# Optimization experiments

Hardware: AMD Instinct MI355X
Metric: run time of the kernel (lower is better)

The kernel has to match this reference:

```python
import jax, jax.numpy as jnp
import numpy as np

E = 8      # num routed experts
H = 1024   # hidden_size
I = 1408   # moe_intermediate_size
T = 2048   # tokens (batch*seq flattened)
K = 2      # top_k experts per token


def setup_inputs() -> dict:
    key = jax.random.key(0)
    k1, k2, k3, k4, k5 = jax.random.split(key, 5)
    x = jax.random.normal(k1, (T, H), dtype=jnp.float32)
    expert_ids = jax.random.randint(k2, (T, K), 0, E, dtype=jnp.int64)
    routing_weights = jax.random.uniform(k3, (T, K), dtype=jnp.float32)
    # kaiming_uniform_(a=sqrt(5)) on 2D tensor -> bound = 1/sqrt(fan_in), fan_in = dim1
    b1 = 1.0 / np.sqrt(2 * I)
    w1 = jax.random.uniform(k4, (E * H, 2 * I), dtype=jnp.float32, minval=-b1, maxval=b1)
    b2 = 1.0 / np.sqrt(H)
    w2 = jax.random.uniform(k5, (E * I, H), dtype=jnp.float32, minval=-b2, maxval=b2)
    return {"x": x, "expert_ids": expert_ids, "routing_weights": routing_weights,
            "w1": w1, "w2": w2}


def reference(x, expert_ids, routing_weights, w1, w2):
    # Fused routed MLP: per token, for each of its top-k experts e with gate p:
    #   out += p * (silu(x @ W1_gate[e]) * (x @ W1_up[e])) @ W2[e]
    w1r = w1.reshape(E, H, 2 * I)   # fused gate+up per expert
    w2r = w2.reshape(E, I, H)       # down proj per expert

    h = jnp.einsum('th,ehi->eti', x, w1r)           # [E, T, 2I]
    gate, up = h[..., :I], h[..., I:]
    act = jax.nn.silu(gate) * up                    # [E, T, I]
    y = jnp.einsum('eti,eih->eth', act, w2r)        # [E, T, H]

    # combine weights: [T, E] = sum over the k slots of onehot(expert)*routing_weight
    disp = jnp.sum(jax.nn.one_hot(expert_ids, E, dtype=x.dtype)
                   * routing_weights[..., None], axis=1)  # [T, E]
    out = jnp.einsum('eth,te->th', y, disp)         # [T, H]
    return out
```

## Files before the change

kernel.cpp:

```cpp
#include <hip/hip_runtime.h>
#include <hip/hip_bf16.h>
#include <math.h>

#define E    8
#define H    1024
#define I2   2816
#define II   1408
#define T    2048
#define KTOP 2
#define NP   (T * KTOP)

#define BM   128
#define BK   32
#define BNA  64
#define BN2  128
#define GX   40
#define GXT  8

#define CVT_BLKS  1024
#define W1_TILES  (16 * 44 * E)
#define PREP_BLKS (1 + CVT_BLKS + W1_TILES)

#define W2_TILES     2816
#define W2_BLOCKS    (GXT * 22)
#define W2_PER_BLOCK (W2_TILES / W2_BLOCKS)

typedef __attribute__((ext_vector_type(8))) short  short8v;
typedef __attribute__((ext_vector_type(4))) float  f32x4;
typedef __attribute__((ext_vector_type(8))) unsigned short ushort8;

__device__ __forceinline__ void gload16(void* lds, const void* g) {
    __builtin_amdgcn_global_load_lds((const __attribute__((address_space(1))) unsigned int*)g,
                                     (__attribute__((address_space(3))) unsigned int*)lds,
                                     16, 0, 0);
}

__device__ __forceinline__ void transpose_tile_async(
    const float* __restrict__ src, __hip_bfloat16* __restrict__ dst,
    int K, int N, int k0, int n0, float* tile, int tid)
{
    int lane = tid & 63;
    int wv   = tid >> 6;
#pragma unroll
    for (int i = 0; i < 4; ++i) {
        int q   = (wv * 4 + i) * 64 + lane;
        int r   = q >> 4;
        int c16 = q & 15;
        const float* gsrc = src + (size_t)(k0 + r) * N + n0 + ((c16 ^ (r & 15)) << 2);
        gload16(tile + q * 4, gsrc);
    }
    __syncthreads();

    int n  = tid >> 2;
    int ks = (tid & 3) * 16;
    alignas(16) __hip_bfloat16 t[16];
#pragma unroll
    for (int j = 0; j < 16; ++j) {
        int r = ks + j;
        float v = tile[r * 64 + (((n >> 2) ^ (r & 15)) << 2) + (n & 3)];
        t[j] = __float2bfloat16(v);
    }
    __hip_bfloat16* d = dst + (size_t)(n0 + n) * K + k0 + ks;
    *(ushort8*)(d)     = ((ushort8*)t)[0];
    *(ushort8*)(d + 8) = ((ushort8*)t)[1];
}

union PrepShared {
    float tile[4096];
    struct { int cnt4[4][E]; int woff[4][E]; } rt;
};

__launch_bounds__(256)
__global__ void prep_kernel(const float* __restrict__ x, const float* __restrict__ w1,
                            const int* __restrict__ ids,
                            __hip_bfloat16* __restrict__ xb,
                            __hip_bfloat16* __restrict__ w1t,
                            int* __restrict__ tok, int* __restrict__ inv,
                            int* __restrict__ seg_off, int* __restrict__ tile_off)
{
    __shared__ __align__(16) PrepShared sh;
    int tid = threadIdx.x;
    int b = blockIdx.x;

    if (b == 0) {
        int lane = tid & 63;
        int w    = tid >> 6;
        unsigned long long ltm = (1ull << lane) - 1ull;

        int wc = 0;
#pragma unroll 1
        for (int it = 0; it < 16; ++it) {
            int p = it * 256 + w * 64 + lane;
            int e = ids[p];
#pragma unroll
            for (int ee = 0; ee < E; ++ee) {
                unsigned long long m = __ballot(e == ee);
                if (lane == ee) wc += (int)__popcll(m);
            }
        }
        if (lane < E) sh.rt.cnt4[w][lane] = wc;
        __syncthreads();
        if (tid == 0) {
            int base = 0, tiles = 0;
            for (int e = 0; e < E; ++e) {
                seg_off[e]  = base;
                tile_off[e] = tiles;
                int tot = 0;
                for (int ww = 0; ww < 4; ++ww) {
                    sh.rt.woff[ww][e] = base + tot;
                    tot += sh.rt.cnt4[ww][e];
                }
                base  += tot;
                tiles += (tot + BM - 1) / BM;
            }
            seg_off[E]  = base;
            tile_off[E] = tiles;
        }
        __syncthreads();
        int run = (lane < E) ? sh.rt.woff[w][lane] : 0;
#pragma unroll 1
        for (int it = 0; it < 16; ++it) {
            int p = it * 256 + w * 64 + lane;
            int e = ids[p];
            unsigned long long me = 0;
            int acnt = 0;
#pragma unroll
            for (int ee = 0; ee < E; ++ee) {
                unsigned long long m = __ballot(e == ee);
                if (e == ee) me = m;
                if (lane == ee) acnt = (int)__popcll(m);
            }
            int rank = (int)__popcll(me & ltm);
            int qb   = __shfl(run, e, 64);
            int q    = qb + rank;
            tok[q] = p >> 1;
            inv[p] = q;
            run += acnt;
        }
        return;
    }
    b -= 1;

    if (b < CVT_BLKS) {
        int i = (b * 256 + tid) * 8;
        float4 a = *(const float4*)(x + i);
        float4 c = *(const float4*)(x + i + 4);
        alignas(16) __hip_bfloat16 t[8];
        t[0] = __float2bfloat16(a.x); t[1] = __float2bfloat16(a.y);
        t[2] = __float2bfloat16(a.z); t[3] = __float2bfloat16(a.w);
        t[4] = __float2bfloat16(c.x); t[5] = __float2bfloat16(c.y);
        t[6] = __float2bfloat16(c.z); t[7] = __float2bfloat16(c.w);
        *(ushort8*)(xb + i) = *(ushort8*)t;
        return;
    }
    b -= CVT_BLKS;

    {
        int e = b / 704, r = b % 704;
        int k0 = (r / 44) * 64, n0 = (r % 44) * 64;
        transpose_tile_async(w1 + (size_t)e * H * I2, w1t + (size_t)e * I2 * H,
                             H, I2, k0, n0, sh.tile, tid);
    }
}

union Gemm1Shared {
    struct {
        __hip_bfloat16 As[BM * BK];
        __hip_bfloat16 Bg[BNA * BK];
        __hip_bfloat16 Bu[BNA * BK];
        int tokS[BM];
    } g;
    float tile[4096];
};

__launch_bounds__(256, 2)
__global__ void gemm1_silu(const __hip_bfloat16* __restrict__ xb,
                           const __hip_bfloat16* __restrict__ w1t,
                           const float* __restrict__ w2,
                           __hip_bfloat16* __restrict__ w2t,
                           const int* __restrict__ tok,
                           const int* __restrict__ seg_off,
                           const int* __restrict__ tile_off,
                           __hip_bfloat16* __restrict__ act)
{
    __shared__ __align__(16) Gemm1Shared sh;
    int tid = threadIdx.x;
    int bx = blockIdx.x;

    if (bx >= GX) {
        int wid = (bx - GX) * 22 + blockIdx.y;
#pragma unroll 1
        for (int i = 0; i < W2_PER_BLOCK; ++i) {
            int t = wid * W2_PER_BLOCK + i;
            int e = t / 352, r = t % 352;
            int k0 = (r >> 4) * 64, n0 = (r & 15) * 64;
            transpose_tile_async(w2 + (size_t)e * II * H, w2t + (size_t)e * H * II,
                                 II, H, k0, n0, sh.tile, tid);
            __syncthreads();
        }
        return;
    }

    if (bx >= tile_off[E]) return;
    int e = 0;
#pragma unroll
    for (int i = 1; i < E; ++i) if (bx >= tile_off[i]) e = i;
    int row0 = seg_off[e] + (bx - tile_off[e]) * BM;
    int rend = seg_off[e + 1];
    int jb   = blockIdx.y * BNA;

    __hip_bfloat16* As = sh.g.As;
    __hip_bfloat16* Bg = sh.g.Bg;
    __hip_bfloat16* Bu = sh.g.Bu;

    if (tid < BM) {
        int gr = row0 + tid;
        sh.g.tokS[tid] = tok[gr < NP ? gr : NP - 1];
    }
    __syncthreads();

    int arow = tid >> 2;
    int aoff = (tid & 3) * 16;
    const char* xB  = (const char*)xb;
    const char* w1B = (const char*)(w1t + (size_t)e * I2 * H);
    const char* srcA0 = xB + (size_t)sh.g.tokS[arow]      * 2048 + aoff;
    const char* srcA1 = xB + (size_t)sh.g.tokS[arow + 64] * 2048 + aoff;
    const char* srcG  = w1B + (size_t)(jb + arow)      * 2048 + aoff;
    const char* srcU  = w1B + (size_t)(II + jb + arow) * 2048 + aoff;
    __hip_bfloat16* dA0 = &As[tid * 8];
    __hip_bfloat16* dA1 = &As[2048 + tid * 8];
    __hip_bfloat16* dG  = &Bg[tid * 8];
    __hip_bfloat16* dU  = &Bu[tid * 8];

    int lane = tid & 63;
    int w  = tid >> 6;
    int wm = w >> 1, wn = w & 1;
    int fr = lane & 15;
    int kc = lane >> 4;

    f32x4 accg[4][2] = {};
    f32x4 accu[4][2] = {};
    const short8v* Asv = (const short8v*)As;
    const short8v* Bgv = (const short8v*)Bg;
    const short8v* Buv = (const short8v*)Bu;

    for (int k0 = 0; k0 < H; k0 += BK) {
        gload16(dA0, srcA0);
        gload16(dA1, srcA1);
        gload16(dG, srcG);
        gload16(dU, srcU);
        srcA0 += 64; srcA1 += 64; srcG += 64; srcU += 64;
        __syncthreads();

        short8v a[4], g[2], u[2];
#pragma unroll
        for (int m = 0; m < 4; ++m)
            a[m] = Asv[(wm * 64 + m * 16 + fr) * 4 + kc];
#pragma unroll
        for (int n = 0; n < 2; ++n) {
            g[n] = Bgv[(wn * 32 + n * 16 + fr) * 4 + kc];
            u[n] = Buv[(wn * 32 + n * 16 + fr) * 4 + kc];
        }
#pragma unroll
        for (int m = 0; m < 4; ++m)
#pragma unroll
            for (int n = 0; n < 2; ++n) {
                accg[m][n] = __builtin_amdgcn_mfma_f32_16x16x32_bf16(a[m], g[n], accg[m][n], 0, 0, 0);
                accu[m][n] = __builtin_amdgcn_mfma_f32_16x16x32_bf16(a[m], u[n], accu[m][n], 0, 0, 0);
            }
        __syncthreads();
    }

#pragma unroll
    for (int m = 0; m < 4; ++m)
#pragma unroll
        for (int n = 0; n < 2; ++n) {
            int col = jb + wn * 32 + n * 16 + fr;
#pragma unroll
            for (int j = 0; j < 4; ++j) {
                int gr = row0 + wm * 64 + m * 16 + kc * 4 + j;
                if (gr < rend) {
                    float gg = accg[m][n][j];
                    float s  = gg / (1.0f + __expf(-gg));
                    act[(size_t)gr * II + col] = __float2bfloat16(s * accu[m][n][j]);
                }
            }
        }
}

__launch_bounds__(256, 2)
__global__ void gemm2(const __hip_bfloat16* __restrict__ act,
                      const __hip_bfloat16* __restrict__ w2t,
                      const int* __restrict__ seg_off,
                      const int* __restrict__ tile_off,
                      float* __restrict__ y)
{
    __shared__ __align__(16) __hip_bfloat16 As[BM * BK];
    __shared__ __align__(16) __hip_bfloat16 Bs[BN2 * BK];

    int bx = blockIdx.x;
    if (bx >= tile_off[E]) return;
    int e = 0;
#pragma unroll
    for (int i = 1; i < E; ++i) if (bx >= tile_off[i]) e = i;
    int row0 = seg_off[e] + (bx - tile_off[e]) * BM;
    int rend = seg_off[e + 1];
    int nb   = blockIdx.y * BN2;

    int tid = threadIdx.x;
    int arow = tid >> 2;
    int aoff = (tid & 3) * 16;
    const char* actB = (const char*)act;
    const char* w2B  = (const char*)(w2t + (size_t)e * H * II);
    int r0c = row0 + arow;       r0c = r0c < NP ? r0c : NP - 1;
    int r1c = row0 + arow + 64;  r1c = r1c < NP ? r1c : NP - 1;
    const char* srcA0 = actB + (size_t)r0c * 2816 + aoff;
    const char* srcA1 = actB + (size_t)r1c * 2816 + aoff;
    const char* srcB0 = w2B + (size_t)(nb + arow)      * 2816 + aoff;
    const char* srcB1 = w2B + (size_t)(nb + arow + 64) * 2816 + aoff;
    __hip_bfloat16* dA0 = &As[tid * 8];
    __hip_bfloat16* dA1 = &As[2048 + tid * 8];
    __hip_bfloat16* dB0 = &Bs[tid * 8];
    __hip_bfloat16* dB1 = &Bs[2048 + tid * 8];

    int lane = tid & 63;
    int w  = tid >> 6;
    int wm = w >> 1, wn = w & 1;
    int fr = lane & 15;
    int kc = lane >> 4;

    f32x4 acc[4][4] = {};
    const short8v* Asv = (const short8v*)As;
    const short8v* Bsv = (const short8v*)Bs;

    for (int k0 = 0; k0 < II; k0 += BK) {
        gload16(dA0, srcA0);
        gload16(dA1, srcA1);
        gload16(dB0, srcB0);
        gload16(dB1, srcB1);
        srcA0 += 64; srcA1 += 64; srcB0 += 64; srcB1 += 64;
        __syncthreads();

        short8v a[4], b[4];
#pragma unroll
        for (int m = 0; m < 4; ++m)
            a[m] = Asv[(wm * 64 + m * 16 + fr) * 4 + kc];
#pragma unroll
        for (int n = 0; n < 4; ++n)
            b[n] = Bsv[(wn * 64 + n * 16 + fr) * 4 + kc];
#pragma unroll
        for (int m = 0; m < 4; ++m)
#pragma unroll
            for (int n = 0; n < 4; ++n)
                acc[m][n] = __builtin_amdgcn_mfma_f32_16x16x32_bf16(a[m], b[n], acc[m][n], 0, 0, 0);
        __syncthreads();
    }

#pragma unroll
    for (int m = 0; m < 4; ++m)
#pragma unroll
        for (int n = 0; n < 4; ++n) {
            int col = nb + wn * 64 + n * 16 + fr;
#pragma unroll
            for (int j = 0; j < 4; ++j) {
                int lr = wm * 64 + m * 16 + kc * 4 + j;
                int gr = row0 + lr;
                if (gr < rend)
                    y[(size_t)gr * H + col] = acc[m][n][j];
            }
        }
}

__global__ void gather_out(const float* __restrict__ y, const int* __restrict__ inv,
                           const float* __restrict__ rw, float* __restrict__ out)
{
    int gid = blockIdx.x * 256 + threadIdx.x;
    int t = gid >> 8;
    int c = (gid & 255) * 4;
    int q0 = inv[2 * t], q1 = inv[2 * t + 1];
    float w0 = rw[2 * t], w1 = rw[2 * t + 1];
    float4 a = *(const float4*)(y + (size_t)q0 * H + c);
    float4 b = *(const float4*)(y + (size_t)q1 * H + c);
    float4 o;
    o.x = w0 * a.x + w1 * b.x;
    o.y = w0 * a.y + w1 * b.y;
    o.z = w0 * a.z + w1 * b.z;
    o.w = w0 * a.w + w1 * b.w;
    *(float4*)(out + (size_t)t * H + c) = o;
}

extern "C" void kernel_launch(void* const* d_in, const int* in_sizes, int n_in,
                              void* d_out, int out_size, void* d_ws, size_t ws_size,
                              hipStream_t stream)
{
    const float* x   = (const float*)d_in[0];
    const int*   ids = (const int*)d_in[1];
    const float* rw  = (const float*)d_in[2];
    const float* w1  = (const float*)d_in[3];
    const float* w2  = (const float*)d_in[4];
    float*       out = (float*)d_out;

    char* ws = (char*)d_ws;
    int*   tok  = (int*)ws;
    int*   inv  = (int*)(ws + 16384);
    int*   seg  = (int*)(ws + 32768);
    int*   tile = (int*)(ws + 32768 + 64);
    __hip_bfloat16* xb  = (__hip_bfloat16*)(ws + 65536);
    __hip_bfloat16* w1t = (__hip_bfloat16*)(ws + 4259840);
    __hip_bfloat16* w2t = (__hip_bfloat16*)(ws + 50397184);
    __hip_bfloat16* act = (__hip_bfloat16*)(ws + 73465856);
    float*          y   = (float*)(ws + 85000192);

    prep_kernel<<<PREP_BLKS, 256, 0, stream>>>(x, w1, ids, xb, w1t, tok, inv, seg, tile);

    gemm1_silu<<<dim3(GX + GXT, II / BNA), 256, 0, stream>>>(xb, w1t, w2, w2t,
                                                             tok, seg, tile, act);
    gemm2<<<dim3(GX, H / BN2), 256, 0, stream>>>(act, w2t, seg, tile, y);
    gather_out<<<(T * H) / (256 * 4), 256, 0, stream>>>(y, inv, rw, out);
}
```

Before: 285.3 us.

## Double-buffer LDS tiles with async prefetch in GEMMs and weight transposes

Converts the gemm1, gemm2 and w2-transpose loops to double-buffered LDS staging. The next k-slice is issued with global_load_lds before the current one is consumed, using s_waitcnt vmcnt(4) and a raw barrier instead of __syncthreads. The prep kernel now handles two W1 transpose tiles per block so the second load overlaps the first tile's processing. The aim is to hide global-load latency behind MFMA and convert work. The cost is double the LDS footprint, which can lower occupancy. Correctness also depends on hand-counted vmcnt values matching the compiler's load ordering.

```diff
diff --git a/kernel.cpp b/kernel.cpp
--- a/kernel.cpp
+++ b/kernel.cpp
@@ -17,9 +17,10 @@
 #define GX   40
 #define GXT  8
 
-#define CVT_BLKS  1024
-#define W1_TILES  (16 * 44 * E)
-#define PREP_BLKS (1 + CVT_BLKS + W1_TILES)
+#define CVT_BLKS   1024
+#define W1_TILES   (16 * 44 * E)
+#define W1_BLKS    (W1_TILES / 2)
+#define PREP_BLKS  (1 + CVT_BLKS + W1_BLKS)
 
 #define W2_TILES     2816
 #define W2_BLOCKS    (GXT * 22)
@@ -28,6 +29,10 @@
 typedef __attribute__((ext_vector_type(8))) short  short8v;
 typedef __attribute__((ext_vector_type(4))) float  f32x4;
 typedef __attribute__((ext_vector_type(8))) unsigned short ushort8;
+
+#define VMCNT4() asm volatile("s_waitcnt vmcnt(4)" ::: "memory")
+#define VMCNT0() asm volatile("s_waitcnt vmcnt(0)" ::: "memory")
+#define BAR()    __builtin_amdgcn_s_barrier()
 
 __device__ __forceinline__ void gload16(void* lds, const void* g) {
     __builtin_amdgcn_global_load_lds((const __attribute__((address_space(1))) unsigned int*)g,
@@ -35,9 +40,8 @@
                                      16, 0, 0);
 }
 
-__device__ __forceinline__ void transpose_tile_async(
-    const float* __restrict__ src, __hip_bfloat16* __restrict__ dst,
-    int K, int N, int k0, int n0, float* tile, int tid)
+__device__ __forceinline__ void tr_issue(const float* __restrict__ src, int N,
+                                         int k0, int n0, float* tile, int tid)
 {
     int lane = tid & 63;
     int wv   = tid >> 6;
@@ -46,19 +50,21 @@
         int q   = (wv * 4 + i) * 64 + lane;
         int r   = q >> 4;
         int c16 = q & 15;
-        const float* gsrc = src + (size_t)(k0 + r) * N + n0 + ((c16 ^ (r & 15)) << 2);
-        gload16(tile + q * 4, gsrc);
-    }
-    __syncthreads();
-
+        gload16(tile + q * 4, src + (size_t)(k0 + r) * N + n0 + ((c16 ^ (r & 15)) << 2));
+    }
+}
+
+__device__ __forceinline__ void tr_process(const float* tile,
+                                           __hip_bfloat16* __restrict__ dst,
+                                           int K, int k0, int n0, int tid)
+{
     int n  = tid >> 2;
     int ks = (tid & 3) * 16;
     alignas(16) __hip_bfloat16 t[16];
 #pragma unroll
     for (int j = 0; j < 16; ++j) {
         int r = ks + j;
-        float v = tile[r * 64 + (((n >> 2) ^ (r & 15)) << 2) + (n & 3)];
-        t[j] = __float2bfloat16(v);
+        t[j] = __float2bfloat16(tile[r * 64 + (((n >> 2) ^ (r & 15)) << 2) + (n & 3)]);
     }
     __hip_bfloat16* d = dst + (size_t)(n0 + n) * K + k0 + ks;
     *(ushort8*)(d)     = ((ushort8*)t)[0];
@@ -66,7 +72,7 @@
 }
 
 union PrepShared {
-    float tile[4096];
+    float tile[2][4096];
     struct { int cnt4[4][E]; int woff[4][E]; } rt;
 };
 
@@ -156,21 +162,34 @@
     b -= CVT_BLKS;
 
     {
-        int e = b / 704, r = b % 704;
-        int k0 = (r / 44) * 64, n0 = (r % 44) * 64;
-        transpose_tile_async(w1 + (size_t)e * H * I2, w1t + (size_t)e * I2 * H,
-                             H, I2, k0, n0, sh.tile, tid);
+        int t0 = b * 2, t1 = b * 2 + 1;
+        int e0 = t0 / 704, r0 = t0 % 704;
+        int e1 = t1 / 704, r1 = t1 % 704;
+        const float*    s0 = w1  + (size_t)e0 * H * I2;
+        const float*    s1 = w1  + (size_t)e1 * H * I2;
+        __hip_bfloat16* d0 = w1t + (size_t)e0 * I2 * H;
+        __hip_bfloat16* d1 = w1t + (size_t)e1 * I2 * H;
+        int k00 = (r0 / 44) * 64, n00 = (r0 % 44) * 64;
+        int k01 = (r1 / 44) * 64, n01 = (r1 % 44) * 64;
+        tr_issue(s0, I2, k00, n00, sh.tile[0], tid);
+        tr_issue(s1, I2, k01, n01, sh.tile[1], tid);
+        VMCNT4();
+        BAR();
+        tr_process(sh.tile[0], d0, H, k00, n00, tid);
+        VMCNT0();
+        BAR();
+        tr_process(sh.tile[1], d1, H, k01, n01, tid);
     }
 }
 
 union Gemm1Shared {
     struct {
-        __hip_bfloat16 As[BM * BK];
-        __hip_bfloat16 Bg[BNA * BK];
-        __hip_bfloat16 Bu[BNA * BK];
+        __hip_bfloat16 As[2][BM * BK];
+        __hip_bfloat16 Bg[2][BNA * BK];
+        __hip_bfloat16 Bu[2][BNA * BK];
         int tokS[BM];
     } g;
-    float tile[4096];
+    float tile[2][4096];
 };
 
 __launch_bounds__(256, 2)
@@ -189,14 +208,33 @@
 
     if (bx >= GX) {
         int wid = (bx - GX) * 22 + blockIdx.y;
+        int tbase = wid * W2_PER_BLOCK;
+        {
+            int t = tbase;
+            int e = t / 352, r = t % 352;
+            tr_issue(w2 + (size_t)e * II * H, H, (r >> 4) * 64, (r & 15) * 64,
+                     sh.tile[0], tid);
+        }
 #pragma unroll 1
         for (int i = 0; i < W2_PER_BLOCK; ++i) {
-            int t = wid * W2_PER_BLOCK + i;
-            int e = t / 352, r = t % 352;
-            int k0 = (r >> 4) * 64, n0 = (r & 15) * 64;
-            transpose_tile_async(w2 + (size_t)e * II * H, w2t + (size_t)e * H * II,
-                                 II, H, k0, n0, sh.tile, tid);
-            __syncthreads();
+            int cur = i & 1;
+            if (i < W2_PER_BLOCK - 1) {
+                int t = tbase + i + 1;
+                int e = t / 352, r = t % 352;
+                tr_issue(w2 + (size_t)e * II * H, H, (r >> 4) * 64, (r & 15) * 64,
+                         sh.tile[cur ^ 1], tid);
+                VMCNT4();
+            } else {
+                VMCNT0();
+            }
+            BAR();
+            {
+                int t = tbase + i;
+                int e = t / 352, r = t % 352;
+                tr_process(sh.tile[cur], w2t + (size_t)e * H * II, II,
+                           (r >> 4) * 64, (r & 15) * 64, tid);
+            }
+            BAR();
         }
         return;
     }
@@ -208,10 +246,6 @@
     int row0 = seg_off[e] + (bx - tile_off[e]) * BM;
     int rend = seg_off[e + 1];
     int jb   = blockIdx.y * BNA;
-
-    __hip_bfloat16* As = sh.g.As;
-    __hip_bfloat16* Bg = sh.g.Bg;
-    __hip_bfloat16* Bu = sh.g.Bu;
 
     if (tid < BM) {
         int gr = row0 + tid;
@@ -227,10 +261,6 @@
     const char* srcA1 = xB + (size_t)sh.g.tokS[arow + 64] * 2048 + aoff;
     const char* srcG  = w1B + (size_t)(jb + arow)      * 2048 + aoff;
     const char* srcU  = w1B + (size_t)(II + jb + arow) * 2048 + aoff;
-    __hip_bfloat16* dA0 = &As[tid * 8];
-    __hip_bfloat16* dA1 = &As[2048 + tid * 8];
-    __hip_bfloat16* dG  = &Bg[tid * 8];
-    __hip_bfloat16* dU  = &Bu[tid * 8];
 
     int lane = tid & 63;
     int w  = tid >> 6;
@@ -240,18 +270,31 @@
 
     f32x4 accg[4][2] = {};
     f32x4 accu[4][2] = {};
-    const short8v* Asv = (const short8v*)As;
-    const short8v* Bgv = (const short8v*)Bg;
-    const short8v* Buv = (const short8v*)Bu;
-
-    for (int k0 = 0; k0 < H; k0 += BK) {
-        gload16(dA0, srcA0);
-        gload16(dA1, srcA1);
-        gload16(dG, srcG);
-        gload16(dU, srcU);
-        srcA0 += 64; srcA1 += 64; srcG += 64; srcU += 64;
-        __syncthreads();
-
+
+    gload16(&sh.g.As[0][tid * 8], srcA0);
+    gload16(&sh.g.As[0][2048 + tid * 8], srcA1);
+    gload16(&sh.g.Bg[0][tid * 8], srcG);
+    gload16(&sh.g.Bu[0][tid * 8], srcU);
+    srcA0 += 64; srcA1 += 64; srcG += 64; srcU += 64;
+
+#pragma unroll 1
+    for (int t = 0; t < H / BK; ++t) {
+        int cur = t & 1;
+        if (t < H / BK - 1) {
+            gload16(&sh.g.As[cur ^ 1][tid * 8], srcA0);
+            gload16(&sh.g.As[cur ^ 1][2048 + tid * 8], srcA1);
+            gload16(&sh.g.Bg[cur ^ 1][tid * 8], srcG);
+            gload16(&sh.g.Bu[cur ^ 1][tid * 8], srcU);
+            srcA0 += 64; srcA1 += 64; srcG += 64; srcU += 64;
+            VMCNT4();
+        } else {
+            VMCNT0();
+        }
+        BAR();
+
+        const short8v* Asv = (const short8v*)sh.g.As[cur];
+        const short8v* Bgv = (const short8v*)sh.g.Bg[cur];
+        const short8v* Buv = (const short8v*)sh.g.Bu[cur];
         short8v a[4], g[2], u[2];
 #pragma unroll
         for (int m = 0; m < 4; ++m)
@@ -268,7 +311,7 @@
                 accg[m][n] = __builtin_amdgcn_mfma_f32_16x16x32_bf16(a[m], g[n], accg[m][n], 0, 0, 0);
                 accu[m][n] = __builtin_amdgcn_mfma_f32_16x16x32_bf16(a[m], u[n], accu[m][n], 0, 0, 0);
             }
-        __syncthreads();
+        BAR();
     }
 
 #pragma unroll
@@ -295,8 +338,8 @@
                       const int* __restrict__ tile_off,
                       float* __restrict__ y)
 {
-    __shared__ __align__(16) __hip_bfloat16 As[BM * BK];
-    __shared__ __align__(16) __hip_bfloat16 Bs[BN2 * BK];
+    __shared__ __align__(16) __hip_bfloat16 As[2][BM * BK];
+    __shared__ __align__(16) __hip_bfloat16 Bs[2][BN2 * BK];
 
     int bx = blockIdx.x;
     if (bx >= tile_off[E]) return;
@@ -318,10 +361,6 @@
     const char* srcA1 = actB + (size_t)r1c * 2816 + aoff;
     const char* srcB0 = w2B + (size_t)(nb + arow)      * 2816 + aoff;
     const char* srcB1 = w2B + (size_t)(nb + arow + 64) * 2816 + aoff;
-    __hip_bfloat16* dA0 = &As[tid * 8];
-    __hip_bfloat16* dA1 = &As[2048 + tid * 8];
-    __hip_bfloat16* dB0 = &Bs[tid * 8];
-    __hip_bfloat16* dB1 = &Bs[2048 + tid * 8];
 
     int lane = tid & 63;
     int w  = tid >> 6;
@@ -330,17 +369,30 @@
     int kc = lane >> 4;
 
     f32x4 acc[4][4] = {};
-    const short8v* Asv = (const short8v*)As;
-    const short8v* Bsv = (const short8v*)Bs;
-
-    for (int k0 = 0; k0 < II; k0 += BK) {
-        gload16(dA0, srcA0);
-        gload16(dA1, srcA1);
-        gload16(dB0, srcB0);
-        gload16(dB1, srcB1);
-        srcA0 += 64; srcA1 += 64; srcB0 += 64; srcB1 += 64;
-        __syncthreads();
-
+
+    gload16(&As[0][tid * 8], srcA0);
+    gload16(&As[0][2048 + tid * 8], srcA1);
+    gload16(&Bs[0][tid * 8], srcB0);
+    gload16(&Bs[0][2048 + tid * 8], srcB1);
+    srcA0 += 64; srcA1 += 64; srcB0 += 64; srcB1 += 64;
+
+#pragma unroll 1
+    for (int t = 0; t < II / BK; ++t) {
+        int cur = t & 1;
+        if (t < II / BK - 1) {
+            gload16(&As[cur ^ 1][tid * 8], srcA0);
+            gload16(&As[cur ^ 1][2048 + tid * 8], srcA1);
+            gload16(&Bs[cur ^ 1][tid * 8], srcB0);
+            gload16(&Bs[cur ^ 1][2048 + tid * 8], srcB1);
+            srcA0 += 64; srcA1 += 64; srcB0 += 64; srcB1 += 64;
+            VMCNT4();
+        } else {
+            VMCNT0();
+        }
+        BAR();
+
+        const short8v* Asv = (const short8v*)As[cur];
+        const short8v* Bsv = (const short8v*)Bs[cur];
         short8v a[4], b[4];
 #pragma unroll
         for (int m = 0; m < 4; ++m)
@@ -353,7 +405,7 @@
 #pragma unroll
             for (int n = 0; n < 4; ++n)
                 acc[m][n] = __builtin_amdgcn_mfma_f32_16x16x32_bf16(a[m], b[n], acc[m][n], 0, 0, 0);
-        __syncthreads();
+        BAR();
     }
 
 #pragma unroll
```

After: 288.6 us. Within noise of the previous version (+1.2%).
